# Kernel optimization log

Measured on AMD Instinct MI355X. Metric: run time of the kernel, lower is better.

## Reference

```python
import jax, jax.numpy as jnp
import numpy as np

B_GRAPHS = 16
N_PER_GRAPH = 128
N_NODES = B_GRAPHS * N_PER_GRAPH  # 2048
HIDDEN = 256
N_HEADS = 8
HEAD_DIM = HIDDEN // N_HEADS
N_LAYERS = 4
K_RPE = 4
N_EDGES = 32768
NUM_NODE_FEATS = 32
NUM_EDGE_TYPES = 16
MAX_DEGREE = 100
MLP_HID = HIDDEN // 2


def _layernorm(x, s, b):
    m = x.mean(-1, keepdims=True)
    v = jnp.var(x, axis=-1, keepdims=True)
    return (x - m) / jnp.sqrt(v + 1e-5) * s + b


def setup_inputs() -> dict:
    key = jax.random.key(0)
    ks = jax.random.split(key, 24)
    s = 0.02
    x_idx = jax.random.randint(ks[0], (N_NODES,), 0, NUM_NODE_FEATS)
    # edges are intra-graph (the torch code drops cross-graph edges)
    src = jax.random.randint(ks[1], (N_EDGES,), 0, N_NODES)
    dst = (src // N_PER_GRAPH) * N_PER_GRAPH + jax.random.randint(ks[2], (N_EDGES,), 0, N_PER_GRAPH)
    edge_index = jnp.stack([src, dst])
    edge_attr = jax.random.randint(ks[3], (N_EDGES,), 0, NUM_EDGE_TYPES)
    batch = jnp.repeat(jnp.arange(B_GRAPHS), N_PER_GRAPH)
    L = N_LAYERS
    return {
        'x_idx': x_idx, 'edge_index': edge_index, 'edge_attr': edge_attr, 'batch': batch,
        'node_emb': jax.random.normal(ks[4], (NUM_NODE_FEATS, HIDDEN)) * s,
        'edge_emb': jax.random.normal(ks[5], (NUM_EDGE_TYPES, N_HEADS)) * s,
        'degree_emb': jax.random.normal(ks[6], (MAX_DEGREE + 1, HIDDEN)) * s,
        'rpe_W1': jax.random.normal(ks[7], (K_RPE + 1, MLP_HID)) * s,
        'rpe_b1': jnp.zeros((MLP_HID,)),
        'rpe_W2': jax.random.normal(ks[8], (MLP_HID, N_HEADS)) * s,
        'rpe_b2': jnp.zeros((N_HEADS,)),
        'Wq': jax.random.normal(ks[9], (L, HIDDEN, HIDDEN)) * s, 'bq': jnp.zeros((L, HIDDEN)),
        'Wk': jax.random.normal(ks[10], (L, HIDDEN, HIDDEN)) * s, 'bk': jnp.zeros((L, HIDDEN)),
        'Wv': jax.random.normal(ks[11], (L, HIDDEN, HIDDEN)) * s, 'bv': jnp.zeros((L, HIDDEN)),
        'Wo': jax.random.normal(ks[12], (L, HIDDEN, HIDDEN)) * s, 'bo': jnp.zeros((L, HIDDEN)),
        'ln1_s': jnp.ones((L, HIDDEN)), 'ln1_b': jnp.zeros((L, HIDDEN)),
        'ln2_s': jnp.ones((L, HIDDEN)), 'ln2_b': jnp.zeros((L, HIDDEN)),
        'ff_W1': jax.random.normal(ks[13], (L, HIDDEN, 2 * HIDDEN)) * s, 'ff_b1': jnp.zeros((L, 2 * HIDDEN)),
        'ff_W2': jax.random.normal(ks[14], (L, 2 * HIDDEN, HIDDEN)) * s, 'ff_b2': jnp.zeros((L, HIDDEN)),
    }


def _forward(x_idx, edge_index, edge_attr, batch,
             node_emb, edge_emb, degree_emb, rpe_W1, rpe_b1, rpe_W2, rpe_b2,
             Wq, bq, Wk, bk, Wv, bv, Wo, bo, ln1_s, ln1_b, ln2_s, ln2_b,
             ff_W1, ff_b1, ff_W2, ff_b2):
    B, n, H, N = B_GRAPHS, N_PER_GRAPH, N_HEADS, N_NODES
    x = node_emb[x_idx]                               # [N, d]
    src, dst = edge_index[0], edge_index[1]
    # degrees from source endpoints (scatter_add in torch)
    deg = jnp.zeros((N,), jnp.int32).at[src].add(1)
    deg_c = jnp.minimum(deg, MAX_DEGREE)

    # ---- RRWP + edge-type attention bias, block-diagonal over graphs ----
    g = batch[src]
    intra = (batch[src] == batch[dst])                # torch code skips cross-graph edges
    u = src % n
    v = dst % n
    intra_f = intra.astype(jnp.float32)
    inv_du = intra_f / jnp.maximum(deg[src], 1).astype(jnp.float32)
    inv_dv = intra_f / jnp.maximum(deg[dst], 1).astype(jnp.float32)
    # random-walk transition matrix per graph [B, n, n]
    T = (jnp.zeros((B, n, n), jnp.float32)
         .at[g, u, v].add(inv_du)
         .at[g, v, u].add(inv_dv))
    # symmetric edge-type bias per graph [B, n, n, H]
    ev = edge_emb[edge_attr] * intra_f[:, None]
    EB = (jnp.zeros((B, n, n, H), jnp.float32)
          .at[g, u, v].add(ev)
          .at[g, v, u].add(ev))
    # walk powers I, T, T^2, ..., T^K -> [B, n, n, K+1]
    I = jnp.broadcast_to(jnp.eye(n, dtype=jnp.float32), (B, n, n))
    powers = [I, T]
    cur = T
    for _ in range(2, K_RPE + 1):
        cur = cur @ T
        powers.append(cur)
    walk = jnp.stack(powers, axis=-1)
    pair = jax.nn.relu(walk @ rpe_W1 + rpe_b1) @ rpe_W2 + rpe_b2   # [B, n, n, H]
    block = (pair + EB).transpose(0, 3, 1, 2)                      # [B, H, n, n]
    ib = jnp.arange(B)
    full = jnp.full((H, B, n, B, n), -jnp.inf, jnp.float32)
    full = full.at[:, ib, :, ib, :].set(block)                     # diag blocks
    attn_bias = full.reshape(H, N, N)

    # ---- transformer stack ----
    deg_vec = degree_emb[deg_c]
    scale = 1.0 / jnp.sqrt(jnp.float32(HEAD_DIM))
    for l in range(N_LAYERS):
        x = x + deg_vec
        Q = (x @ Wq[l] + bq[l]).reshape(N, H, HEAD_DIM)
        K_ = (x @ Wk[l] + bk[l]).reshape(N, H, HEAD_DIM)
        V = (x @ Wv[l] + bv[l]).reshape(N, H, HEAD_DIM)
        scores = jnp.einsum('ihd,jhd->hij', Q, K_) * scale + attn_bias
        aw = jax.nn.softmax(scores, axis=-1)
        out = jnp.einsum('hij,jhd->ihd', aw, V).reshape(N, HIDDEN)
        out = out @ Wo[l] + bo[l]
        x = _layernorm(x + out, ln1_s[l], ln1_b[l])
        ff = jax.nn.relu(x @ ff_W1[l] + ff_b1[l]) @ ff_W2[l] + ff_b2[l]
        x = _layernorm(x + ff, ln2_s[l], ln2_b[l])
    # global add pool
    return jax.ops.segment_sum(x, batch, num_segments=B)


def reference(x_idx, edge_index, edge_attr, batch,
              node_emb, edge_emb, degree_emb, rpe_W1, rpe_b1, rpe_W2, rpe_b2,
              Wq, bq, Wk, bk, Wv, bv, Wo, bo, ln1_s, ln1_b, ln2_s, ln2_b,
              ff_W1, ff_b1, ff_W2, ff_b2):
    return _forward(x_idx, edge_index, edge_attr, batch,
                    node_emb, edge_emb, degree_emb, rpe_W1, rpe_b1, rpe_W2, rpe_b2,
                    Wq, bq, Wk, bk, Wv, bv, Wo, bo, ln1_s, ln1_b, ln2_s, ln2_b,
                    ff_W1, ff_b1, ff_W2, ff_b2)
```

## Files before the change

kernel.cpp:

```cpp
#include <hip/hip_runtime.h>
#include <hip/hip_bf16.h>

#define B_GRAPHS 16
#define NPG 128
#define NN 2048
#define HIDDEN 256
#define N_HEADS 8
#define HEAD_DIM 32
#define N_LAYERS 4
#define N_EDGES 32768
#define MLP_HID 128
#define MAX_DEG 100

typedef __hip_bfloat16 bf16;
typedef unsigned short ushort_t;
typedef __attribute__((ext_vector_type(8))) short short8;
typedef __attribute__((ext_vector_type(4))) float f32x4;

__device__ __forceinline__ float us2f(ushort_t u) {
    return __uint_as_float(((unsigned)u) << 16);
}
__device__ __forceinline__ ushort_t f2us(float f) {
    unsigned u = __float_as_uint(f);
    return (ushort_t)((u + 0x7FFFu + ((u >> 16) & 1u)) >> 16);
}
__device__ __forceinline__ bool is_bf16_mode(const unsigned* probe) {
    return probe[0] != 0x3F800000u;
}
#define MFMA16(a, b, c) __builtin_amdgcn_mfma_f32_16x16x32_bf16(a, b, c, 0, 0, 0)

__device__ __forceinline__ void gload_lds16(const void* g, void* l) {
    __builtin_amdgcn_global_load_lds(
        (const __attribute__((address_space(1))) unsigned int*)g,
        (__attribute__((address_space(3))) unsigned int*)l, 16, 0, 0);
}
#define SBAR __builtin_amdgcn_s_barrier()
#define WAITP8 asm volatile("s_waitcnt vmcnt(8) lgkmcnt(0)" ::: "memory")
#define WAITLAST asm volatile("s_waitcnt vmcnt(0) lgkmcnt(0)" ::: "memory")
#define LBAR do { asm volatile("s_waitcnt lgkmcnt(0)" ::: "memory"); SBAR; \
                  asm volatile("" ::: "memory"); } while (0)

#define NW 23
__device__ const int c_wsizes[NW] = {
    8192, 128, 25856, 640, 128, 1024, 8,
    262144, 1024, 262144, 1024, 262144, 1024, 262144, 1024,
    1024, 1024, 1024, 1024,
    524288, 2048, 524288, 1024};
#define TOTW 2144392

#define OFF_NODE_EMB 0
#define OFF_EDGE_EMB 8192
#define OFF_DEG_EMB  8320
#define OFF_RPE_W1   34176
#define OFF_RPE_B1   34816
#define OFF_RPE_W2   34944
#define OFF_RPE_B2   35968
#define OFF_BO       1087624
#define OFF_LN1S     1088648
#define OFF_LN1B     1089672
#define OFF_LN2S     1090696
#define OFF_LN2B     1091720
#define OFF_FFB1     1617032
#define OFF_FFB2     2143368

#define WB_QKV 0
#define WB_O   786432
#define WB_F1  1048576
#define WB_F2  1572864
#define WB_TOT 2097152
#define QKVB_TOT 3072

#define ZERO_BLKS 2306
#define CONV_BLKS 8389
#define TP_BLKS   2048

struct SrcPtrs { const void* p[NW]; };

__global__ __launch_bounds__(256) void prep1(SrcPtrs sp, const unsigned* __restrict__ probe,
                                             float* __restrict__ Wc, float* __restrict__ qkvb,
                                             f32x4* __restrict__ zerop,
                                             ushort_t* __restrict__ WB) {
    __shared__ float tile[32][33];
    int b = blockIdx.x;
    bool isbf = is_bf16_mode(probe);
    auto rd = [&](int seg, int off) -> float {
        return isbf ? us2f(((const ushort_t*)sp.p[seg])[off])
                    : ((const float*)sp.p[seg])[off];
    };
    if (b < ZERO_BLKS) {
        f32x4 z;
        z[0] = 0.f; z[1] = 0.f; z[2] = 0.f; z[3] = 0.f;
        zerop[b * 256 + threadIdx.x] = z;
    } else if (b < ZERO_BLKS + CONV_BLKS) {
        int i = (b - ZERO_BLKS) * 256 + threadIdx.x;
        if (i < TOTW) {
            int seg = 0, off = i;
            while (seg < NW - 1 && off >= c_wsizes[seg]) { off -= c_wsizes[seg]; seg++; }
            Wc[i] = rd(seg, off);
        } else if (i < TOTW + QKVB_TOT) {
            int j = i - TOTW;
            int l = j / 768, n = j % 768, which = n >> 8, nn = n & 255;
            int seg = (which == 0) ? 8 : (which == 1) ? 10 : 12;
            qkvb[j] = rd(seg, l * 256 + nn);
        }
    } else {
        int tb = b - ZERO_BLKS - CONV_BLKS;
        int seg, soff, srcN, k0, n0, dK;
        size_t doff;
        if (tb < 768) {
            int mat = tb >> 6, t = tb & 63;
            int l = mat / 3, which = mat % 3;
            seg = 7 + which * 2;
            soff = l * 65536; srcN = 256;
            k0 = (t >> 3) * 32; n0 = (t & 7) * 32;
            doff = (size_t)l * 196608 + (size_t)which * 65536; dK = 256;
        } else if (tb < 1024) {
            int u = tb - 768, l = u >> 6, t = u & 63;
            seg = 13; soff = l * 65536; srcN = 256;
            k0 = (t >> 3) * 32; n0 = (t & 7) * 32;
            doff = WB_O + (size_t)l * 65536; dK = 256;
        } else if (tb < 1536) {
            int u = tb - 1024, l = u >> 7, t = u & 127;
            seg = 19; soff = l * 131072; srcN = 512;
            k0 = (t >> 4) * 32; n0 = (t & 15) * 32;
            doff = WB_F1 + (size_t)l * 131072; dK = 256;
        } else {
            int u = tb - 1536, l = u >> 7, t = u & 127;
            seg = 21; soff = l * 131072; srcN = 256;
            k0 = (t >> 3) * 32; n0 = (t & 7) * 32;
            doff = WB_F2 + (size_t)l * 131072; dK = 512;
        }
        int xcol = threadIdx.x & 31, y8 = threadIdx.x >> 5;
        const void* srcp = sp.p[seg];
#pragma unroll
        for (int rr = 0; rr < 4; rr++) {
            int row = y8 * 4 + rr;
            int off = soff + (k0 + row) * srcN + n0 + xcol;
            tile[row][xcol] = isbf ? us2f(((const ushort_t*)srcp)[off])
                                   : ((const float*)srcp)[off];
        }
        __syncthreads();
#pragma unroll
        for (int rr = 0; rr < 4; rr++) {
            int nrow = y8 * 4 + rr;
            WB[doff + (size_t)(n0 + nrow) * dK + k0 + xcol] = f2us(tile[xcol][nrow]);
        }
    }
}

__global__ void deg_kernel(const int* __restrict__ src, int* __restrict__ deg) {
    int e = blockIdx.x * blockDim.x + threadIdx.x;
    if (e < N_EDGES) atomicAdd(&deg[src[e]], 1);
}

__global__ void prep2(const int* __restrict__ xidx, const int* __restrict__ deg,
                      const float* __restrict__ emb, const float* __restrict__ demb,
                      float* __restrict__ x, ushort_t* __restrict__ xb,
                      const int* __restrict__ ei, const int* __restrict__ eattr,
                      const int* __restrict__ batch, const float* __restrict__ edge_emb,
                      float* __restrict__ T, float* __restrict__ bias) {
    int b = blockIdx.x;
    if (b < 2048) {
        int i = b * 256 + threadIdx.x;
        int node = i >> 8, c = i & 255;
        float v = emb[xidx[node] * HIDDEN + c] + demb[min(deg[node], MAX_DEG) * HIDDEN + c];
        x[i] = v;
        xb[i] = f2us(v);
    } else {
        int idx = (b - 2048) * 256 + threadIdx.x;
        int e = idx >> 3, h = idx & 7;
        int s = ei[e], d = ei[N_EDGES + e];
        if (batch[s] != batch[d]) return;
        int g = batch[s];
        int u = s & (NPG - 1), v = d & (NPG - 1);
        if (h == 0) {
            atomicAdd(&T[(g * NPG + u) * NPG + v], 1.0f / (float)max(deg[s], 1));
            atomicAdd(&T[(g * NPG + v) * NPG + u], 1.0f / (float)max(deg[d], 1));
        }
        float ev = edge_emb[eattr[e] * N_HEADS + h];
        atomicAdd(&bias[(((size_t)(g * N_HEADS + h) * NPG + u) * NPG + v)], ev);
        atomicAdd(&bias[(((size_t)(g * N_HEADS + h) * NPG + v) * NPG + u)], ev);
    }
}

__global__ void matmul128(const float* __restrict__ A, const float* __restrict__ B,
                          float* __restrict__ C) {
    int g = blockIdx.x / NPG;
    int row = blockIdx.x % NPG;
    int col = threadIdx.x;
    const float* Ag = A + (size_t)g * NPG * NPG;
    const float* Bg = B + (size_t)g * NPG * NPG;
    __shared__ float arow[NPG];
    arow[col] = Ag[row * NPG + col];
    __syncthreads();
    float acc = 0.f;
#pragma unroll 8
    for (int k = 0; k < NPG; k++) acc += arow[k] * Bg[k * NPG + col];
    C[((size_t)g * NPG + row) * NPG + col] = acc;
}

__global__ void matmul128_dual(const float* __restrict__ T2, const float* __restrict__ T,
                               float* __restrict__ T3, float* __restrict__ T4) {
    int half = blockIdx.x >> 11;
    int bid = blockIdx.x & 2047;
    int g = bid / NPG, row = bid % NPG, col = threadIdx.x;
    const float* Ag = T2 + (size_t)g * NPG * NPG;
    const float* Bg = (half ? T2 : T) + (size_t)g * NPG * NPG;
    float* Cg = (half ? T4 : T3) + (size_t)g * NPG * NPG;
    __shared__ float arow[NPG];
    arow[col] = Ag[row * NPG + col];
    __syncthreads();
    float acc = 0.f;
#pragma unroll 8
    for (int k = 0; k < NPG; k++) acc += arow[k] * Bg[k * NPG + col];
    Cg[row * NPG + col] = acc;
}

__global__ __launch_bounds__(256) void rpe_kernel(
    const float* __restrict__ T, const float* __restrict__ T2,
    const float* __restrict__ T3, const float* __restrict__ T4,
    const float* __restrict__ W1, const float* __restrict__ b1,
    const float* __restrict__ W2, const float* __restrict__ b2,
    float* __restrict__ bias) {
    __shared__ float sW1[5][MLP_HID];
    __shared__ float sb1[MLP_HID];
    __shared__ float sW2[MLP_HID][N_HEADS];
    int t = threadIdx.x;
    for (int i = t; i < 5 * MLP_HID; i += 256) sW1[i / MLP_HID][i % MLP_HID] = W1[i];
    for (int i = t; i < MLP_HID; i += 256) sb1[i] = b1[i];
    for (int i = t; i < MLP_HID * N_HEADS; i += 256) sW2[i / N_HEADS][i % N_HEADS] = W2[i];
    __syncthreads();
    int p = blockIdx.x * 256 + t;
    int g = p / (NPG * NPG);
    int rem = p % (NPG * NPG);
    int i = rem / NPG, j = rem % NPG;
    float f0 = (i == j) ? 1.f : 0.f;
    float f1 = T[p], f2 = T2[p], f3 = T3[p], f4 = T4[p];
    float acc[N_HEADS];
#pragma unroll
    for (int h = 0; h < N_HEADS; h++) acc[h] = b2[h];
#pragma unroll 4
    for (int m = 0; m < MLP_HID; m++) {
        float hv = sb1[m] + f0 * sW1[0][m] + f1 * sW1[1][m] + f2 * sW1[2][m] +
                   f3 * sW1[3][m] + f4 * sW1[4][m];
        hv = fmaxf(hv, 0.f);
#pragma unroll
        for (int h = 0; h < N_HEADS; h++) acc[h] += hv * sW2[m][h];
    }
#pragma unroll
    for (int h = 0; h < N_HEADS; h++)
        bias[(((size_t)(g * N_HEADS + h) * NPG + i) * NPG + j)] += acc[h];
}

__global__ __launch_bounds__(256, 1) void qkv_attn(
    const ushort_t* __restrict__ x_bf, const ushort_t* __restrict__ WT,
    const float* __restrict__ qb, const float* __restrict__ bias,
    ushort_t* __restrict__ ao) {
    int bid = blockIdx.x;
    int g = bid >> 4, h = (bid >> 1) & 7, half = bid & 1;
    int wave = threadIdx.x >> 6, lane = threadIdx.x & 63;
    int lr = lane & 15, lq = lane >> 4;

    __shared__ char Wbuf[3][16384];
    __shared__ ushort_t Qs[64][40];
    __shared__ ushort_t Ks[NPG][40];
    __shared__ ushort_t VT[32][136];
    __shared__ ushort_t P[4][16][136];

    const ushort_t* xg = x_bf + (size_t)g * NPG * HIDDEN;
    int qrow = half * 64 + wave * 16;
    int kvrow = wave * 32;

    short8 Aq[8], Akv[2][8];
#pragma unroll
    for (int kk = 0; kk < 8; kk++) {
        Aq[kk] = *(const short8*)(xg + (size_t)(qrow + lr) * 256 + kk * 32 + lq * 8);
#pragma unroll
        for (int i = 0; i < 2; i++)
            Akv[i][kk] = *(const short8*)(xg + (size_t)(kvrow + i * 16 + lr) * 256 +
                                          kk * 32 + lq * 8);
    }
    float bqv[2], bkv[2], bvv[2];
#pragma unroll
    for (int j = 0; j < 2; j++) {
        int c = h * 32 + j * 16 + lr;
        bqv[j] = qb[c]; bkv[j] = qb[256 + c]; bvv[j] = qb[512 + c];
    }
    asm volatile("s_waitcnt vmcnt(0) lgkmcnt(0)" ::: "memory");

    auto stageW = [&](int rowbase, int c) {
        const char* gW = (const char*)WT;
        char* lb = &Wbuf[c][0] + wave * 4096;
#pragma unroll
        for (int it = 0; it < 4; it++) {
            int j = wave * 4096 + it * 1024 + lane * 16;
            int n = j >> 9, off = j & 511;
            gload_lds16(gW + (size_t)(rowbase + n) * 512 + (off ^ ((n & 7) << 4)),
                        lb + it * 1024);
        }
        __builtin_amdgcn_sched_barrier(0);
    };
    stageW(h * 32, 0);
    stageW(256 + h * 32, 1);
    stageW(512 + h * 32, 2);

    const float* bg = bias + (size_t)(g * N_HEADS + h) * NPG * NPG;
    float bgv[8][4];
#pragma unroll
    for (int r = 0; r < 4; r++) {
        int i = half * 64 + wave * 16 + lq * 4 + r;
#pragma unroll
        for (int jt = 0; jt < 8; jt++)
            bgv[jt][r] = bg[(size_t)i * NPG + jt * 16 + lr];
    }
    __builtin_amdgcn_sched_barrier(0);

    auto rdW = [&](int c, int jt, int kk) -> short8 {
        int n = jt * 16 + lr;
        int off = n * 512 + ((kk * 64 + lq * 16) ^ ((n & 7) << 4));
        return *(const short8*)(&Wbuf[c][off]);
    };

    f32x4 qa[2]{}, ka[2][2]{}, va[2][2]{};
    asm volatile("s_waitcnt vmcnt(40)" ::: "memory"); SBAR;
#pragma unroll
    for (int kk = 0; kk < 8; kk++)
#pragma unroll
        for (int j = 0; j < 2; j++)
            qa[j] = MFMA16(Aq[kk], rdW(0, j, kk), qa[j]);

    asm volatile("s_waitcnt vmcnt(36)" ::: "memory"); SBAR;
#pragma unroll
    for (int kk = 0; kk < 8; kk++)
#pragma unroll
        for (int j = 0; j < 2; j++)
#pragma unroll
            for (int i = 0; i < 2; i++)
                ka[i][j] = MFMA16(Akv[i][kk], rdW(1, j, kk), ka[i][j]);

    asm volatile("s_waitcnt vmcnt(32)" ::: "memory"); SBAR;
#pragma unroll
    for (int kk = 0; kk < 8; kk++)
#pragma unroll
        for (int j = 0; j < 2; j++)
#pragma unroll
            for (int i = 0; i < 2; i++)
                va[i][j] = MFMA16(Akv[i][kk], rdW(2, j, kk), va[i][j]);

#pragma unroll
    for (int j = 0; j < 2; j++) {
        int c = j * 16 + lr;
#pragma unroll
        for (int r = 0; r < 4; r++) {
            Qs[wave * 16 + lq * 4 + r][c] = f2us(qa[j][r] + bqv[j]);
#pragma unroll
            for (int i = 0; i < 2; i++) {
                int row = kvrow + i * 16 + lq * 4 + r;
                Ks[row][c] = f2us(ka[i][j][r] + bkv[j]);
                VT[c][row] = f2us(va[i][j][r] + bvv[j]);
            }
        }
    }
    __syncthreads();

    short8 qf = *(const short8*)(&Qs[wave * 16 + lr][lq * 8]);
    f32x4 S[8];
    f32x4 zero;
    zero[0] = 0.f; zero[1] = 0.f; zero[2] = 0.f; zero[3] = 0.f;
#pragma unroll
    for (int jt = 0; jt < 8; jt++) {
        short8 kf = *(const short8*)(&Ks[jt * 16 + lr][lq * 8]);
        S[jt] = MFMA16(qf, kf, zero);
    }

    const float scale = 0.17677669529663687f;
    float lrow[4];
#pragma unroll
    for (int r = 0; r < 4; r++) {
        float mx = -1e30f;
#pragma unroll
        for (int jt = 0; jt < 8; jt++) {
            float s = S[jt][r] * scale + bgv[jt][r];
            S[jt][r] = s;
            mx = fmaxf(mx, s);
        }
#pragma unroll
        for (int m = 1; m < 16; m <<= 1) mx = fmaxf(mx, __shfl_xor(mx, m));
        float sum = 0.f;
#pragma unroll
        for (int jt = 0; jt < 8; jt++) {
            float e = __expf(S[jt][r] - mx);
            S[jt][r] = e;
            sum += e;
        }
#pragma unroll
        for (int m = 1; m < 16; m <<= 1) sum += __shfl_xor(sum, m);
        lrow[r] = sum;
    }

#pragma unroll
    for (int jt = 0; jt < 8; jt++)
#pragma unroll
        for (int r = 0; r < 4; r++)
            P[wave][lq * 4 + r][jt * 16 + lr] = f2us(S[jt][r]);

    f32x4 O[2]{};
#pragma unroll
    for (int k0 = 0; k0 < NPG; k0 += 32) {
        short8 pa = *(const short8*)(&P[wave][lr][k0 + lq * 8]);
#pragma unroll
        for (int dt = 0; dt < 2; dt++) {
            short8 vb = *(const short8*)(&VT[dt * 16 + lr][k0 + lq * 8]);
            O[dt] = MFMA16(pa, vb, O[dt]);
        }
    }
#pragma unroll
    for (int r = 0; r < 4; r++) {
        float inv = 1.f / lrow[r];
        int row = g * NPG + half * 64 + wave * 16 + lq * 4 + r;
#pragma unroll
        for (int dt = 0; dt < 2; dt++)
            ao[(size_t)row * HIDDEN + h * 32 + dt * 16 + lr] = f2us(O[dt][r] * inv);
    }
}

__global__ __launch_bounds__(512, 2) void fused_mlp(
    const ushort_t* __restrict__ ao, const ushort_t* __restrict__ WoT,
    const float* __restrict__ bo, const float* __restrict__ ln1s,
    const float* __restrict__ ln1b,
    const ushort_t* __restrict__ F1T, const ushort_t* __restrict__ F2T,
    const float* __restrict__ fb1, const float* __restrict__ fb2,
    const float* __restrict__ ln2s, const float* __restrict__ ln2b,
    const float* __restrict__ xin, const int* __restrict__ deg,
    const float* __restrict__ demb, int add_deg,
    float* __restrict__ xout, ushort_t* __restrict__ xb) {
    int m0 = blockIdx.x * 8;
    int wave = threadIdx.x >> 6, lane = threadIdx.x & 63;
    int lr = lane & 15, lq = lane >> 4;
    int ar = m0 + (lr & 7);

    __shared__ ushort_t Wbuf[2][32768];
    __shared__ ushort_t xs_bf[8][264];
    __shared__ ushort_t ffh[8][520];
    __shared__ float ws[8][16], qs[8][16];

    auto stageO = [&](int h, int b) {
        const char* gW = (const char*)WoT;
        char* lb = (char*)&Wbuf[b][0] + wave * 8192;
#pragma unroll
        for (int it = 0; it < 8; it++) {
            int j = wave * 8192 + it * 1024 + lane * 16;
            int n = j >> 8, off = j & 255;
            gload_lds16(gW + n * 512 + h * 256 + (off ^ ((n & 7) << 4)), lb + it * 1024);
        }
        __builtin_amdgcn_sched_barrier(0);
    };
    auto stageF1 = [&](int q, int b) {
        const char* gW = (const char*)F1T;
        char* lb = (char*)&Wbuf[b][0] + wave * 8192;
#pragma unroll
        for (int it = 0; it < 8; it++) {
            int j = wave * 8192 + it * 1024 + lane * 16;
            int n = j >> 9, off = j & 511;
            gload_lds16(gW + (q * 128 + n) * 512 + (off ^ ((n & 7) << 4)), lb + it * 1024);
        }
        __builtin_amdgcn_sched_barrier(0);
    };
    auto stageF2 = [&](int q, int b) {
        const char* gW = (const char*)F2T;
        char* lb = (char*)&Wbuf[b][0] + wave * 8192;
#pragma unroll
        for (int it = 0; it < 8; it++) {
            int j = wave * 8192 + it * 1024 + lane * 16;
            int n = j >> 8, off = j & 255;
            gload_lds16(gW + n * 1024 + q * 256 + (off ^ ((n & 7) << 4)), lb + it * 1024);
        }
        __builtin_amdgcn_sched_barrier(0);
    };

    float bo_v[2], l1s[2], l1b[2], fb2v[2], l2s[2], l2b[2], xres[2][4], fb1q[4];
#pragma unroll
    for (int jt = 0; jt < 2; jt++) {
        int col = wave * 32 + jt * 16 + lr;
        bo_v[jt] = bo[col]; l1s[jt] = ln1s[col]; l1b[jt] = ln1b[col];
        fb2v[jt] = fb2[col]; l2s[jt] = ln2s[col]; l2b[jt] = ln2b[col];
#pragma unroll
        for (int r = 0; r < 4; r++) {
            int row = m0 + ((lq * 4 + r) & 7);
            xres[jt][r] = xin[(size_t)row * 256 + col];
        }
    }
#pragma unroll
    for (int q = 0; q < 4; q++) fb1q[q] = fb1[q * 128 + wave * 16 + lr];
    int dg4[4];
    if (add_deg) {
#pragma unroll
        for (int r = 0; r < 4; r++)
            dg4[r] = min(deg[m0 + ((lq * 4 + r) & 7)], MAX_DEG);
    }
    short8 Af[8];
#pragma unroll
    for (int t = 0; t < 8; t++)
        Af[t] = *(const short8*)(ao + (size_t)ar * 256 + t * 32 + lq * 8);

    stageO(0, 0);
    stageO(1, 1);

    f32x4 acc[2]{};
#pragma unroll
    for (int h = 0; h < 2; h++) {
        WAITP8; SBAR; asm volatile("" ::: "memory");
#pragma unroll
        for (int kk = 0; kk < 4; kk++) {
            short8 a = Af[h * 4 + kk];
#pragma unroll
            for (int jt = 0; jt < 2; jt++) {
                int n = wave * 32 + jt * 16 + lr;
                int bo_ = n * 256 + ((kk * 64 + lq * 16) ^ ((n & 7) << 4));
                short8 bf = *(const short8*)((const char*)&Wbuf[h][0] + bo_);
                acc[jt] = MFMA16(a, bf, acc[jt]);
            }
        }
        LBAR;
        if (h == 0) stageF1(0, 0);
        else        stageF1(1, 1);
    }

    float valLN[2][4], meanst[4];
#pragma unroll
    for (int r = 0; r < 4; r++) {
        float s = 0.f;
#pragma unroll
        for (int jt = 0; jt < 2; jt++) {
            float v = acc[jt][r] + bo_v[jt] + xres[jt][r];
            valLN[jt][r] = v;
            s += v;
        }
#pragma unroll
        for (int m = 1; m < 16; m <<= 1) s += __shfl_xor(s, m);
        if (lr == 0) ws[wave][lq * 4 + r] = s;
    }
    LBAR;
#pragma unroll
    for (int r = 0; r < 4; r++) {
        int rr = lq * 4 + r;
        float sum = 0.f;
#pragma unroll
        for (int c = 0; c < 8; c++) sum += ws[c][rr];
        float mean = sum * (1.f / 256.f);
        meanst[r] = mean;
        float q = 0.f;
#pragma unroll
        for (int jt = 0; jt < 2; jt++) {
            float d = valLN[jt][r] - mean;
            q += d * d;
        }
#pragma unroll
        for (int m = 1; m < 16; m <<= 1) q += __shfl_xor(q, m);
        if (lr == 0) qs[wave][rr] = q;
    }
    LBAR;
#pragma unroll
    for (int r = 0; r < 4; r++) {
        int rr = lq * 4 + r;
        float qsum = 0.f;
#pragma unroll
        for (int c = 0; c < 8; c++) qsum += qs[c][rr];
        float rstd = rsqrtf(qsum * (1.f / 256.f) + 1e-5f);
#pragma unroll
        for (int jt = 0; jt < 2; jt++) {
            int col = wave * 32 + jt * 16 + lr;
            float y = (valLN[jt][r] - meanst[r]) * rstd * l1s[jt] + l1b[jt];
            valLN[jt][r] = y;
            if (rr < 8) xs_bf[rr][col] = f2us(y);
        }
    }

#pragma unroll
    for (int q = 0; q < 4; q++) {
        WAITP8; SBAR; asm volatile("" ::: "memory");
        f32x4 a1{};
        int nl = wave * 16 + lr;
#pragma unroll
        for (int kk = 0; kk < 8; kk++) {
            short8 a = *(const short8*)(&xs_bf[lr & 7][kk * 32 + lq * 8]);
            int bo_ = nl * 512 + ((kk * 64 + lq * 16) ^ ((nl & 7) << 4));
            short8 bf = *(const short8*)((const char*)&Wbuf[q & 1][0] + bo_);
            a1 = MFMA16(a, bf, a1);
        }
        int col = q * 128 + wave * 16 + lr;
#pragma unroll
        for (int r = 0; r < 4; r++) {
            int rr = lq * 4 + r;
            if (rr < 8) ffh[rr][col] = f2us(fmaxf(a1[r] + fb1q[q], 0.f));
        }
        LBAR;
        if (q < 2) stageF1(q + 2, q & 1);
        else       stageF2(q - 2, q & 1);
    }

    f32x4 acc2[2]{};
#pragma unroll
    for (int q = 0; q < 4; q++) {
        if (q == 3) { WAITLAST; } else { WAITP8; }
        SBAR; asm volatile("" ::: "memory");
#pragma unroll
        for (int kk = 0; kk < 4; kk++) {
            short8 a = *(const short8*)(&ffh[lr & 7][q * 128 + kk * 32 + lq * 8]);
#pragma unroll
            for (int jt = 0; jt < 2; jt++) {
                int n = wave * 32 + jt * 16 + lr;
                int bo_ = n * 256 + ((kk * 64 + lq * 16) ^ ((n & 7) << 4));
                short8 bf = *(const short8*)((const char*)&Wbuf[q & 1][0] + bo_);
                acc2[jt] = MFMA16(a, bf, acc2[jt]);
            }
        }
        LBAR;
        if (q < 2) stageF2(q + 2, q & 1);
    }

    float val2[2][4];
#pragma unroll
    for (int r = 0; r < 4; r++) {
        int rr = lq * 4 + r;
        float s = 0.f;
#pragma unroll
        for (int jt = 0; jt < 2; jt++) {
            float v = acc2[jt][r] + fb2v[jt] + valLN[jt][r];
            val2[jt][r] = v;
            s += v;
        }
#pragma unroll
        for (int m = 1; m < 16; m <<= 1) s += __shfl_xor(s, m);
        if (lr == 0) ws[wave][rr] = s;
    }
    __syncthreads();
#pragma unroll
    for (int r = 0; r < 4; r++) {
        int rr = lq * 4 + r;
        float sum = 0.f;
#pragma unroll
        for (int c = 0; c < 8; c++) sum += ws[c][rr];
        float mean = sum * (1.f / 256.f);
        meanst[r] = mean;
        float q = 0.f;
#pragma unroll
        for (int jt = 0; jt < 2; jt++) {
            float d = val2[jt][r] - mean;
            q += d * d;
        }
#pragma unroll
        for (int m = 1; m < 16; m <<= 1) q += __shfl_xor(q, m);
        if (lr == 0) qs[wave][rr] = q;
    }
    __syncthreads();
#pragma unroll
    for (int r = 0; r < 4; r++) {
        int rr = lq * 4 + r;
        float qsum = 0.f;
#pragma unroll
        for (int c = 0; c < 8; c++) qsum += qs[c][rr];
        float rstd = rsqrtf(qsum * (1.f / 256.f) + 1e-5f);
        if (rr < 8) {
            int row = m0 + rr;
#pragma unroll
            for (int jt = 0; jt < 2; jt++) {
                int col = wave * 32 + jt * 16 + lr;
                float y = (val2[jt][r] - meanst[r]) * rstd * l2s[jt] + l2b[jt];
                if (add_deg) y += demb[dg4[r] * 256 + col];
                xout[(size_t)row * 256 + col] = y;
                xb[(size_t)row * 256 + col] = f2us(y);
            }
        }
    }
}

__global__ void pool_kernel(const float* __restrict__ x, void* __restrict__ out,
                            const unsigned* __restrict__ probe) {
    int b = blockIdx.x;
    int c = threadIdx.x;
    float acc = 0.f;
#pragma unroll 4
    for (int i = 0; i < NPG; i++) acc += x[(size_t)(b * NPG + i) * HIDDEN + c];
    if (is_bf16_mode(probe))
        ((bf16*)out)[b * HIDDEN + c] = __float2bfloat16(acc);
    else
        ((float*)out)[b * HIDDEN + c] = acc;
}

extern "C" void kernel_launch(void* const* d_in, const int* in_sizes, int n_in,
                              void* d_out, int out_size, void* d_ws, size_t ws_size,
                              hipStream_t stream) {
    const int* x_idx      = (const int*)d_in[0];
    const int* edge_index = (const int*)d_in[1];
    const int* edge_attr  = (const int*)d_in[2];
    const int* batch      = (const int*)d_in[3];
    const unsigned* probe = (const unsigned*)d_in[19];

    char* base = (char*)d_ws;
    float* Wc    = (float*)base;       base += (size_t)TOTW * 4;
    float* x     = (float*)base;       base += (size_t)NN * HIDDEN * 4;
    float* T     = (float*)base;       base += 262144 * 4;
    float* bias  = (float*)base;       base += (size_t)2097152 * 4;
    int*   deg   = (int*)base;         base += 2048 * 4;
    float* T2    = (float*)base;       base += 262144 * 4;
    float* T3    = (float*)base;       base += 262144 * 4;
    float* T4    = (float*)base;       base += 262144 * 4;
    float* qkvb  = (float*)base;       base += QKVB_TOT * 4;
    ushort_t* WB    = (ushort_t*)base; base += (size_t)WB_TOT * 2;
    ushort_t* x_bf  = (ushort_t*)base; base += (size_t)NN * HIDDEN * 2;
    ushort_t* ao_bf = (ushort_t*)base; base += (size_t)NN * HIDDEN * 2;

    SrcPtrs sp;
    for (int i = 0; i < NW; i++) sp.p[i] = d_in[4 + i];

    prep1<<<ZERO_BLKS + CONV_BLKS + TP_BLKS, 256, 0, stream>>>(sp, probe, Wc, qkvb,
                                                               (f32x4*)T, WB);
    deg_kernel<<<N_EDGES / 256, 256, 0, stream>>>(edge_index, deg);
    prep2<<<3072, 256, 0, stream>>>(x_idx, deg, Wc + OFF_NODE_EMB, Wc + OFF_DEG_EMB,
                                    x, x_bf, edge_index, edge_attr, batch,
                                    Wc + OFF_EDGE_EMB, T, bias);
    matmul128<<<B_GRAPHS * NPG, NPG, 0, stream>>>(T, T, T2);
    matmul128_dual<<<2 * B_GRAPHS * NPG, NPG, 0, stream>>>(T2, T, T3, T4);
    rpe_kernel<<<(B_GRAPHS * NPG * NPG) / 256, 256, 0, stream>>>(
        T, T2, T3, T4, Wc + OFF_RPE_W1, Wc + OFF_RPE_B1, Wc + OFF_RPE_W2, Wc + OFF_RPE_B2,
        bias);

    for (int l = 0; l < N_LAYERS; l++) {
        qkv_attn<<<2 * B_GRAPHS * N_HEADS, 256, 0, stream>>>(
            x_bf, WB + WB_QKV + (size_t)l * 196608, qkvb + l * 768, bias, ao_bf);
        fused_mlp<<<NN / 8, 512, 0, stream>>>(
            ao_bf, WB + WB_O + (size_t)l * 65536, Wc + OFF_BO + l * 256,
            Wc + OFF_LN1S + l * 256, Wc + OFF_LN1B + l * 256,
            WB + WB_F1 + (size_t)l * 131072, WB + WB_F2 + (size_t)l * 131072,
            Wc + OFF_FFB1 + l * 512, Wc + OFF_FFB2 + l * 256,
            Wc + OFF_LN2S + l * 256, Wc + OFF_LN2B + l * 256, x,
            deg, Wc + OFF_DEG_EMB, (l < N_LAYERS - 1) ? 1 : 0, x, x_bf);
    }
    pool_kernel<<<B_GRAPHS, 256, 0, stream>>>(x, d_out, probe);
}
```

Baseline: 331.9 us.

## Merge half-blocks in qkv_attn so one 512-thread block handles a full graph-head

The attention kernel previously launched two 256-thread blocks per (graph, head), each recomputing the full K and V projections for all 128 nodes while computing Q for only half the rows. It now launches one 512-thread block per (graph, head) where each of 8 waves projects Q, K and V for its own 16 rows, so the K/V projection is done once instead of twice. Q is staged through the per-wave P buffer instead of a separate Qs array. The trade-off is half as many blocks (128 instead of 256), which lowers parallelism on a GPU with many CUs, in exchange for removing the redundant projection work and the duplicate weight staging.

```diff
diff --git a/kernel.cpp b/kernel.cpp
--- a/kernel.cpp
+++ b/kernel.cpp
@@ -252,34 +252,26 @@
         bias[(((size_t)(g * N_HEADS + h) * NPG + i) * NPG + j)] += acc[h];
 }
 
-__global__ __launch_bounds__(256, 1) void qkv_attn(
+__global__ __launch_bounds__(512, 1) void qkv_attn(
     const ushort_t* __restrict__ x_bf, const ushort_t* __restrict__ WT,
     const float* __restrict__ qb, const float* __restrict__ bias,
     ushort_t* __restrict__ ao) {
-    int bid = blockIdx.x;
-    int g = bid >> 4, h = (bid >> 1) & 7, half = bid & 1;
-    int wave = threadIdx.x >> 6, lane = threadIdx.x & 63;
+    int g = blockIdx.x >> 3, h = blockIdx.x & 7;
+    int o = threadIdx.x >> 6, lane = threadIdx.x & 63;
     int lr = lane & 15, lq = lane >> 4;
 
     __shared__ char Wbuf[3][16384];
-    __shared__ ushort_t Qs[64][40];
     __shared__ ushort_t Ks[NPG][40];
     __shared__ ushort_t VT[32][136];
-    __shared__ ushort_t P[4][16][136];
+    __shared__ ushort_t P[8][16][136];
 
     const ushort_t* xg = x_bf + (size_t)g * NPG * HIDDEN;
-    int qrow = half * 64 + wave * 16;
-    int kvrow = wave * 32;
-
-    short8 Aq[8], Akv[2][8];
-#pragma unroll
-    for (int kk = 0; kk < 8; kk++) {
-        Aq[kk] = *(const short8*)(xg + (size_t)(qrow + lr) * 256 + kk * 32 + lq * 8);
-#pragma unroll
-        for (int i = 0; i < 2; i++)
-            Akv[i][kk] = *(const short8*)(xg + (size_t)(kvrow + i * 16 + lr) * 256 +
-                                          kk * 32 + lq * 8);
-    }
+    int row16 = o * 16;
+
+    short8 Ax[8];
+#pragma unroll
+    for (int kk = 0; kk < 8; kk++)
+        Ax[kk] = *(const short8*)(xg + (size_t)(row16 + lr) * 256 + kk * 32 + lq * 8);
     float bqv[2], bkv[2], bvv[2];
 #pragma unroll
     for (int j = 0; j < 2; j++) {
@@ -290,10 +282,10 @@
 
     auto stageW = [&](int rowbase, int c) {
         const char* gW = (const char*)WT;
-        char* lb = &Wbuf[c][0] + wave * 4096;
-#pragma unroll
-        for (int it = 0; it < 4; it++) {
-            int j = wave * 4096 + it * 1024 + lane * 16;
+        char* lb = &Wbuf[c][0] + o * 2048;
+#pragma unroll
+        for (int it = 0; it < 2; it++) {
+            int j = o * 2048 + it * 1024 + lane * 16;
             int n = j >> 9, off = j & 511;
             gload_lds16(gW + (size_t)(rowbase + n) * 512 + (off ^ ((n & 7) << 4)),
                         lb + it * 1024);
@@ -308,7 +300,7 @@
     float bgv[8][4];
 #pragma unroll
     for (int r = 0; r < 4; r++) {
-        int i = half * 64 + wave * 16 + lq * 4 + r;
+        int i = row16 + lq * 4 + r;
 #pragma unroll
         for (int jt = 0; jt < 8; jt++)
             bgv[jt][r] = bg[(size_t)i * NPG + jt * 16 + lr];
@@ -321,49 +313,42 @@
         return *(const short8*)(&Wbuf[c][off]);
     };
 
-    f32x4 qa[2]{}, ka[2][2]{}, va[2][2]{};
-    asm volatile("s_waitcnt vmcnt(40)" ::: "memory"); SBAR;
+    f32x4 qa[2]{}, ka[2]{}, va[2]{};
+    asm volatile("s_waitcnt vmcnt(36)" ::: "memory"); SBAR;
 #pragma unroll
     for (int kk = 0; kk < 8; kk++)
 #pragma unroll
         for (int j = 0; j < 2; j++)
-            qa[j] = MFMA16(Aq[kk], rdW(0, j, kk), qa[j]);
-
-    asm volatile("s_waitcnt vmcnt(36)" ::: "memory"); SBAR;
+            qa[j] = MFMA16(Ax[kk], rdW(0, j, kk), qa[j]);
+
+    asm volatile("s_waitcnt vmcnt(34)" ::: "memory"); SBAR;
 #pragma unroll
     for (int kk = 0; kk < 8; kk++)
 #pragma unroll
         for (int j = 0; j < 2; j++)
-#pragma unroll
-            for (int i = 0; i < 2; i++)
-                ka[i][j] = MFMA16(Akv[i][kk], rdW(1, j, kk), ka[i][j]);
+            ka[j] = MFMA16(Ax[kk], rdW(1, j, kk), ka[j]);
 
     asm volatile("s_waitcnt vmcnt(32)" ::: "memory"); SBAR;
 #pragma unroll
     for (int kk = 0; kk < 8; kk++)
 #pragma unroll
         for (int j = 0; j < 2; j++)
-#pragma unroll
-            for (int i = 0; i < 2; i++)
-                va[i][j] = MFMA16(Akv[i][kk], rdW(2, j, kk), va[i][j]);
+            va[j] = MFMA16(Ax[kk], rdW(2, j, kk), va[j]);
 
 #pragma unroll
     for (int j = 0; j < 2; j++) {
         int c = j * 16 + lr;
 #pragma unroll
         for (int r = 0; r < 4; r++) {
-            Qs[wave * 16 + lq * 4 + r][c] = f2us(qa[j][r] + bqv[j]);
-#pragma unroll
-            for (int i = 0; i < 2; i++) {
-                int row = kvrow + i * 16 + lq * 4 + r;
-                Ks[row][c] = f2us(ka[i][j][r] + bkv[j]);
-                VT[c][row] = f2us(va[i][j][r] + bvv[j]);
-            }
+            int row = row16 + lq * 4 + r;
+            P[o][lq * 4 + r][c] = f2us(qa[j][r] + bqv[j]);
+            Ks[row][c] = f2us(ka[j][r] + bkv[j]);
+            VT[c][row] = f2us(va[j][r] + bvv[j]);
         }
     }
     __syncthreads();
 
-    short8 qf = *(const short8*)(&Qs[wave * 16 + lr][lq * 8]);
+    short8 qf = *(const short8*)(&P[o][lr][lq * 8]);
     f32x4 S[8];
     f32x4 zero;
     zero[0] = 0.f; zero[1] = 0.f; zero[2] = 0.f; zero[3] = 0.f;
@@ -402,12 +387,12 @@
     for (int jt = 0; jt < 8; jt++)
 #pragma unroll
         for (int r = 0; r < 4; r++)
-            P[wave][lq * 4 + r][jt * 16 + lr] = f2us(S[jt][r]);
+            P[o][lq * 4 + r][jt * 16 + lr] = f2us(S[jt][r]);
 
     f32x4 O[2]{};
 #pragma unroll
     for (int k0 = 0; k0 < NPG; k0 += 32) {
-        short8 pa = *(const short8*)(&P[wave][lr][k0 + lq * 8]);
+        short8 pa = *(const short8*)(&P[o][lr][k0 + lq * 8]);
 #pragma unroll
         for (int dt = 0; dt < 2; dt++) {
             short8 vb = *(const short8*)(&VT[dt * 16 + lr][k0 + lq * 8]);
@@ -417,7 +402,7 @@
 #pragma unroll
     for (int r = 0; r < 4; r++) {
         float inv = 1.f / lrow[r];
-        int row = g * NPG + half * 64 + wave * 16 + lq * 4 + r;
+        int row = g * NPG + row16 + lq * 4 + r;
 #pragma unroll
         for (int dt = 0; dt < 2; dt++)
             ao[(size_t)row * HIDDEN + h * 32 + dt * 16 + lr] = f2us(O[dt][r] * inv);
@@ -727,7 +712,7 @@
         bias);
 
     for (int l = 0; l < N_LAYERS; l++) {
-        qkv_attn<<<2 * B_GRAPHS * N_HEADS, 256, 0, stream>>>(
+        qkv_attn<<<B_GRAPHS * N_HEADS, 512, 0, stream>>>(
             x_bf, WB + WB_QKV + (size_t)l * 196608, qkvb + l * 768, bias, ao_bf);
         fused_mlp<<<NN / 8, 512, 0, stream>>>(
             ao_bf, WB + WB_O + (size_t)l * 65536, Wc + OFF_BO + l * 256,
```

New measurement: 329.7 us. Within noise of the previous version (-0.7%).
